# Performance work log

Hardware: AMD Instinct MI355X
Metric: run time of the kernel (lower is better)

Reference implementation:

```python
import jax, jax.numpy as jnp
import numpy as np

# Graph layout: B equal-sized graphs, contiguous node ids.
B, NG, EG = 64, 2000, 64000          # graphs, nodes/graph, edges/graph
K = 1600                              # ceil(0.8 * NG) — TopKPooling ratio=0.8
N, E = B * NG, B * EG
FEAT_DIM, EMB, G1, G2, DENSE, NCLS = 10000, 64, 32, 32, 64, 10


def setup_inputs() -> dict:
    key = jax.random.key(0)
    ks = jax.random.split(key, 12)
    x = jax.random.randint(ks[0], (N, 1), 0, FEAT_DIM)
    # random edges within each graph, then offset by graph base node id
    e = jax.random.randint(ks[1], (2, B, EG), 0, NG) + (jnp.arange(B) * NG)[None, :, None]
    edge_index = e.reshape(2, E)
    batch = jnp.repeat(jnp.arange(B), NG)
    sc = 0.05
    return {
        "x": x, "edge_index": edge_index, "batch": batch,
        "emb": jax.random.normal(ks[2], (FEAT_DIM, EMB), jnp.float32) * sc,
        "W1": jax.random.normal(ks[3], (EMB, G1), jnp.float32) * sc,
        "b1": jnp.zeros((G1,), jnp.float32),
        "W2": jax.random.normal(ks[4], (G1, G2), jnp.float32) * sc,
        "b2": jnp.zeros((G2,), jnp.float32),
        "pool_w": jax.random.normal(ks[5], (G2,), jnp.float32) * sc,
        "dense_W": jax.random.normal(ks[6], (G2, DENSE), jnp.float32) * sc,
        "dense_b": jnp.zeros((DENSE,), jnp.float32),
        "out_W": jax.random.normal(ks[7], (DENSE, NCLS), jnp.float32) * sc,
        "out_b": jnp.zeros((NCLS,), jnp.float32),
    }


def gcn_layer(h, src, dst, W, b):
    """PyG GCNConv: add self-loops, symmetric D^-1/2 A D^-1/2 aggregation."""
    n = h.shape[0]
    loop = jnp.arange(n)
    s = jnp.concatenate([src, loop])
    d = jnp.concatenate([dst, loop])
    h = h @ W                                                   # [N, out]
    deg = jax.ops.segment_sum(jnp.ones_like(d, dtype=h.dtype), d, num_segments=n)
    dinv = jnp.where(deg > 0, deg ** -0.5, 0.0)
    norm = dinv[s] * dinv[d]                                    # [E+N]
    out = jax.ops.segment_sum(h[s] * norm[:, None], d, num_segments=n)
    return out + b


def reference(x, edge_index, batch, emb, W1, b1, W2, b2, pool_w,
              dense_W, dense_b, out_W, out_b):
    h = emb[x[:, 0]]                                            # [N, EMB]
    src, dst = edge_index[0], edge_index[1]
    h = jax.nn.relu(gcn_layer(h, src, dst, W1, b1))
    h = jax.nn.relu(gcn_layer(h, src, dst, W2, b2))
    # TopKPooling: score = tanh(x.w / ||w||); keep top ceil(0.8*NG) per graph,
    # scale kept features by their scores. Equal graph sizes -> static shapes.
    score = jnp.tanh(h @ pool_w / jnp.linalg.norm(pool_w))      # [N]
    sb = score.reshape(B, NG)
    hb = h.reshape(B, NG, G2)
    vals, idx = jax.lax.top_k(sb, K)                            # [B, K]
    hp = jnp.take_along_axis(hb, idx[:, :, None], axis=1) * vals[:, :, None]
    g = hp.max(axis=1)                                          # global max pool [B, G2]
    d = jax.nn.relu(g @ dense_W + dense_b)
    return d @ out_W + out_b                                    # [B, NCLS]
```

## Files before the change

### kernel.cpp

```cpp
#include <hip/hip_runtime.h>
#include <hip/hip_fp16.h>
#include <math.h>

#define NB 64
#define NGRAPH 2000
#define EGRAPH 64000
#define NN (NB*NGRAPH)
#define NE (NB*EGRAPH)
#define KSEL 1600
#define FEAT 10000
#define EMBD 64
#define G1D 32
#define G2D 32
#define DENSED 64
#define NCLSD 10
#define NCHUNK 8
#define CHUNK_E (EGRAPH/NCHUNK)
#define NQD 8
#define QNODES (NGRAPH/NQD)
#define LOUT_CAP 10000
#define AGG_PARTS 4
#define NPP (NGRAPH/AGG_PARTS)


__device__ __forceinline__ float4 ld_row8h(const char* base, unsigned byteoff)
{
    uint2 u = *(const uint2*)(base + byteoff);
    __half2 p0 = *(__half2*)&u.x;
    __half2 p1 = *(__half2*)&u.y;
    float2 f0 = __half22float2(p0);
    float2 f1 = __half22float2(p1);
    return make_float4(f0.x, f0.y, f1.x, f1.y);
}

__device__ __forceinline__ void st_row8h(__half* dst, float4 v)
{
    __half2 p0 = __floats2half2_rn(v.x, v.y);
    __half2 p1 = __floats2half2_rn(v.z, v.w);
    uint2 u;
    u.x = *(unsigned*)&p0;
    u.y = *(unsigned*)&p1;
    *(uint2*)dst = u;
}

__global__ __launch_bounds__(256) void prep_kernel(const int* __restrict__ ei,
                                                   int* __restrict__ chist,
                                                   const float* __restrict__ emb,
                                                   const float* __restrict__ W1,
                                                   float* __restrict__ embW)
{
    __shared__ float shmem[2048];
    const int tid = threadIdx.x;
    if (blockIdx.x < 512) {
        int* hist = (int*)shmem;
        const int lb = blockIdx.x;
        const int xcd = lb & 7, t = lb >> 3;
        const int g = xcd * 8 + (t >> 3);
        const int q = t & 7;
        const int base_e = g * EGRAPH + q * CHUNK_E;
        const int base_n = g * NGRAPH;
        for (int v = tid; v < NGRAPH; v += 256) hist[v] = 0;
        __syncthreads();
        for (int k = tid; k < CHUNK_E; k += 256) {
            int d = ei[NE + base_e + k];
            atomicAdd(&hist[d - base_n], 1);
        }
        __syncthreads();
        int* out = chist + (size_t)(g * NCHUNK + q) * NGRAPH;
        for (int v = tid; v < NGRAPH; v += 256) out[v] = hist[v];
    } else {
        float* W1s = shmem;
        for (int i = tid; i < EMBD * G1D; i += 256) W1s[i] = W1[i];
        __syncthreads();
        int id = (blockIdx.x - 512) * 256 + tid;
        int r = id >> 5, c = id & 31;
        if (r >= FEAT) return;
        const float* er = emb + r * EMBD;
        float acc = 0.f;
        #pragma unroll 8
        for (int k = 0; k < EMBD; ++k) acc += er[k] * W1s[k * G1D + c];
        embW[r * G1D + c] = acc;
    }
}

__global__ __launch_bounds__(256) void scan_graph(const int* __restrict__ chist,
                                                  float* __restrict__ dinv,
                                                  int* __restrict__ row_start)
{
    __shared__ int hist[NGRAPH];
    __shared__ int csA[256];
    __shared__ int csB[256];
    const int b = (blockIdx.x & 7) * 8 + (blockIdx.x >> 3);
    const int tid = threadIdx.x;
    const int base_n = b * NGRAPH, base_e = b * EGRAPH;
    const int* ch = chist + (size_t)b * NCHUNK * NGRAPH;

    for (int v = tid; v < NGRAPH; v += 256) {
        int tot = 0;
        #pragma unroll
        for (int q = 0; q < NCHUNK; ++q) tot += ch[q * NGRAPH + v];
        hist[v] = tot;
        dinv[base_n + v] = rsqrtf((float)(tot + 1));
    }
    __syncthreads();
    if (tid < 250) {
        int s = 0;
        #pragma unroll
        for (int i = 0; i < 8; ++i) s += hist[tid * 8 + i];
        csA[tid] = s;
    }
    __syncthreads();
    int* sb = csA; int* db = csB;
    for (int off = 1; off < 256; off <<= 1) {
        int v = 0;
        if (tid < 250) { v = sb[tid]; if (tid >= off) v += sb[tid - off]; }
        if (tid < 250) db[tid] = v;
        __syncthreads();
        int* t = sb; sb = db; db = t;
    }
    if (tid < 250) {
        int run = (tid == 0) ? 0 : sb[tid - 1];
        #pragma unroll
        for (int i = 0; i < 8; ++i) {
            int idx = tid * 8 + i;
            int c = hist[idx];
            row_start[base_n + idx] = base_e + run;
            run += c;
        }
    }
}

__global__ __launch_bounds__(1024) void mid_kernel(const int* __restrict__ ei,
                                                   const int* __restrict__ row_start,
                                                   int* __restrict__ csr,
                                                   const int* __restrict__ x,
                                                   const float* __restrict__ embW,
                                                   const float* __restrict__ dinv,
                                                   __half* __restrict__ A)
{
    __shared__ int cur[QNODES];
    __shared__ int lout[LOUT_CAP];
    const int tid = threadIdx.x;
    if (blockIdx.x < 512) {
        const int lb = blockIdx.x;
        const int xcd = lb & 7, t = lb >> 3;
        const int g = xcd * 8 + (t >> 3);
        const int qd = t & 7;
        const int base_n = g * NGRAPH;
        const int lo = qd * QNODES;
        const int base = row_start[base_n + lo];
        const int qend = (g == NB - 1 && qd == NQD - 1) ? NE
                         : row_start[base_n + lo + QNODES];
        for (int v = tid; v < QNODES; v += 1024)
            cur[v] = row_start[base_n + lo + v] - base;
        __syncthreads();
        const int4* srcp = (const int4*)(ei + g * EGRAPH);
        const int4* dstp = (const int4*)(ei + NE + g * EGRAPH);
        const int sub = base_n + lo;
        for (int k = tid; k < EGRAPH / 4; k += 1024) {
            int4 d4 = dstp[k];
            int4 s4 = srcp[k];
            int d, pos;
            d = d4.x - sub;
            if ((unsigned)d < (unsigned)QNODES) {
                pos = atomicAdd(&cur[d], 1);
                if (pos < LOUT_CAP) lout[pos] = s4.x << 6;
            }
            d = d4.y - sub;
            if ((unsigned)d < (unsigned)QNODES) {
                pos = atomicAdd(&cur[d], 1);
                if (pos < LOUT_CAP) lout[pos] = s4.y << 6;
            }
            d = d4.z - sub;
            if ((unsigned)d < (unsigned)QNODES) {
                pos = atomicAdd(&cur[d], 1);
                if (pos < LOUT_CAP) lout[pos] = s4.z << 6;
            }
            d = d4.w - sub;
            if ((unsigned)d < (unsigned)QNODES) {
                pos = atomicAdd(&cur[d], 1);
                if (pos < LOUT_CAP) lout[pos] = s4.w << 6;
            }
        }
        __syncthreads();
        int size = qend - base;
        if (size > LOUT_CAP) size = LOUT_CAP;
        for (int i = tid; i < size; i += 1024)
            csr[base + i] = lout[i];
    } else {
        int id = (blockIdx.x - 512) * 1024 + tid;
        int v = id >> 3, r = id & 7;
        int xv = x[v];
        float dv = dinv[v];
        float4 e = ((const float4*)(embW + (size_t)xv * G1D))[r];
        e.x *= dv; e.y *= dv; e.z *= dv; e.w *= dv;
        st_row8h(A + (size_t)v * G1D + r * 4, e);
    }
}


__global__ __launch_bounds__(1024) void agg1_kernel(const __half* __restrict__ Ain,
                                                    const float* __restrict__ dinv,
                                                    const int* __restrict__ row_start,
                                                    const int* __restrict__ csr,
                                                    const float* __restrict__ b1,
                                                    const float* __restrict__ W2,
                                                    __half* __restrict__ Bout)
{
    __shared__ uint4 table4[NGRAPH * 4];
    __shared__ float hsh[32][G2D];
    const int lb = blockIdx.x;
    const int xcd = lb & 7, t = lb >> 3;
    const int b = xcd * 8 + (t >> 2);
    const int part = t & 3;
    const int tid = threadIdx.x;
    const int base_n = b * NGRAPH;
    const int boff = base_n << 6;

    {
        const uint4* src = (const uint4*)(Ain + (size_t)base_n * G1D);
        for (int i = tid; i < NGRAPH * 4; i += 1024) table4[i] = src[i];
    }
    __syncthreads();

    const char* Lbase = (const char*)table4;
    const int hw = tid >> 5;
    const int hl = tid & 31;
    const int slot = hl >> 3;
    const int r = hl & 7;
    const int roff = r << 3;
    const float4 bias4 = ((const float4*)b1)[r];

    float w2c[G1D];
    #pragma unroll
    for (int k = 0; k < G1D; ++k) w2c[k] = W2[k * G2D + hl];

    const int vloc0 = part * NPP + hw * 16;
    const int vend = part * NPP + NPP;
    int v = base_n + vloc0;
    int rs = row_start[v];
    int re = (v == NN - 1) ? NE : row_start[v + 1];
    int s0 = csr[rs + slot] - boff;
    int s1 = csr[rs + slot + 4] - boff;
    int s2 = csr[rs + slot + 8] - boff;
    int s3 = csr[rs + slot + 12] - boff;

    for (int i = 0; i < 16; ++i) {
        int vloc = vloc0 + i;
        if (vloc >= vend) break;
        int re_next = (v + 1 >= NN - 1) ? NE : row_start[v + 2];
        int n0 = csr[re + slot] - boff;
        int n1 = csr[re + slot + 4] - boff;
        int n2 = csr[re + slot + 8] - boff;
        int n3 = csr[re + slot + 12] - boff;

        int me = rs + ((re - rs) & ~15);
        float4 acc0 = make_float4(0.f, 0.f, 0.f, 0.f);
        float4 acc1 = make_float4(0.f, 0.f, 0.f, 0.f);
        float4 acc2 = make_float4(0.f, 0.f, 0.f, 0.f);
        float4 acc3 = make_float4(0.f, 0.f, 0.f, 0.f);
        if (slot == 0)
            acc0 = ld_row8h(Lbase, (unsigned)((vloc << 6) + roff));
        int j = rs + slot;
        while (j < me) {
            int jn = j + 16;
            int t0 = csr[jn] - boff;
            int t1 = csr[jn + 4] - boff;
            int t2 = csr[jn + 8] - boff;
            int t3 = csr[jn + 12] - boff;
            float4 a0 = ld_row8h(Lbase, (unsigned)(s0 + roff));
            float4 a1 = ld_row8h(Lbase, (unsigned)(s1 + roff));
            float4 a2 = ld_row8h(Lbase, (unsigned)(s2 + roff));
            float4 a3 = ld_row8h(Lbase, (unsigned)(s3 + roff));
            acc0.x += a0.x; acc0.y += a0.y; acc0.z += a0.z; acc0.w += a0.w;
            acc1.x += a1.x; acc1.y += a1.y; acc1.z += a1.z; acc1.w += a1.w;
            acc2.x += a2.x; acc2.y += a2.y; acc2.z += a2.z; acc2.w += a2.w;
            acc3.x += a3.x; acc3.y += a3.y; acc3.z += a3.z; acc3.w += a3.w;
            j = jn; s0 = t0; s1 = t1; s2 = t2; s3 = t3;
        }
        {
            int jt = me + slot;
            if (jt < re) {
                float4 a = ld_row8h(Lbase, (unsigned)(s0 + roff));
                acc0.x += a.x; acc0.y += a.y; acc0.z += a.z; acc0.w += a.w;
            }
            if (jt + 4 < re) {
                float4 a = ld_row8h(Lbase, (unsigned)(s1 + roff));
                acc1.x += a.x; acc1.y += a.y; acc1.z += a.z; acc1.w += a.w;
            }
            if (jt + 8 < re) {
                float4 a = ld_row8h(Lbase, (unsigned)(s2 + roff));
                acc2.x += a.x; acc2.y += a.y; acc2.z += a.z; acc2.w += a.w;
            }
            if (jt + 12 < re) {
                float4 a = ld_row8h(Lbase, (unsigned)(s3 + roff));
                acc3.x += a.x; acc3.y += a.y; acc3.z += a.z; acc3.w += a.w;
            }
        }
        float4 acc;
        acc.x = (acc0.x + acc1.x) + (acc2.x + acc3.x);
        acc.y = (acc0.y + acc1.y) + (acc2.y + acc3.y);
        acc.z = (acc0.z + acc1.z) + (acc2.z + acc3.z);
        acc.w = (acc0.w + acc1.w) + (acc2.w + acc3.w);
        #pragma unroll
        for (int off = 8; off <= 16; off <<= 1) {
            acc.x += __shfl_xor(acc.x, off, 32);
            acc.y += __shfl_xor(acc.y, off, 32);
            acc.z += __shfl_xor(acc.z, off, 32);
            acc.w += __shfl_xor(acc.w, off, 32);
        }
        float dv = dinv[v];
        if (slot == 0) {
            float4 h4;
            h4.x = fmaxf(dv * acc.x + bias4.x, 0.f);
            h4.y = fmaxf(dv * acc.y + bias4.y, 0.f);
            h4.z = fmaxf(dv * acc.z + bias4.z, 0.f);
            h4.w = fmaxf(dv * acc.w + bias4.w, 0.f);
            ((float4*)&hsh[hw][0])[r] = h4;
        }
        float o0 = 0.f, o1 = 0.f, o2 = 0.f, o3 = 0.f;
        const float4* hrow = (const float4*)&hsh[hw][0];
        #pragma unroll
        for (int q = 0; q < 8; ++q) {
            float4 hh = hrow[q];
            o0 += hh.x * w2c[4 * q + 0];
            o1 += hh.y * w2c[4 * q + 1];
            o2 += hh.z * w2c[4 * q + 2];
            o3 += hh.w * w2c[4 * q + 3];
        }
        Bout[(size_t)v * G2D + hl] = __float2half(dv * ((o0 + o1) + (o2 + o3)));
        v = v + 1;
        rs = re; re = re_next; s0 = n0; s1 = n1; s2 = n2; s3 = n3;
    }
}

__global__ __launch_bounds__(1024) void agg2_kernel(const __half* __restrict__ Bin,
                                                    const float* __restrict__ dinv,
                                                    const int* __restrict__ row_start,
                                                    const int* __restrict__ csr,
                                                    const float* __restrict__ b2,
                                                    const float* __restrict__ pool_w,
                                                    __half* __restrict__ h2out,
                                                    float* __restrict__ scores)
{
    __shared__ uint4 table4[NGRAPH * 4];
    const int lb = blockIdx.x;
    const int xcd = lb & 7, t = lb >> 3;
    const int b = xcd * 8 + (t >> 2);
    const int part = t & 3;
    const int tid = threadIdx.x;
    const int base_n = b * NGRAPH;
    const int boff = base_n << 6;

    {
        const uint4* src = (const uint4*)(Bin + (size_t)base_n * G1D);
        for (int i = tid; i < NGRAPH * 4; i += 1024) table4[i] = src[i];
    }
    __syncthreads();

    const char* Lbase = (const char*)table4;
    const int hw = tid >> 5;
    const int hl = tid & 31;
    const int slot = hl >> 3;
    const int r = hl & 7;
    const int roff = r << 3;
    const float4 bias4 = ((const float4*)b2)[r];
    const float4 pw4 = ((const float4*)pool_w)[r];

    float pw = pool_w[hl];
    float nsq = pw * pw;
    #pragma unroll
    for (int off = 16; off; off >>= 1) nsq += __shfl_xor(nsq, off, 32);
    const float inv_norm = rsqrtf(nsq);

    const int vloc0 = part * NPP + hw * 16;
    const int vend = part * NPP + NPP;
    int v = base_n + vloc0;
    int rs = row_start[v];
    int re = (v == NN - 1) ? NE : row_start[v + 1];
    int s0 = csr[rs + slot] - boff;
    int s1 = csr[rs + slot + 4] - boff;
    int s2 = csr[rs + slot + 8] - boff;
    int s3 = csr[rs + slot + 12] - boff;

    for (int i = 0; i < 16; ++i) {
        int vloc = vloc0 + i;
        if (vloc >= vend) break;
        int re_next = (v + 1 >= NN - 1) ? NE : row_start[v + 2];
        int n0 = csr[re + slot] - boff;
        int n1 = csr[re + slot + 4] - boff;
        int n2 = csr[re + slot + 8] - boff;
        int n3 = csr[re + slot + 12] - boff;

        int me = rs + ((re - rs) & ~15);
        float4 acc0 = make_float4(0.f, 0.f, 0.f, 0.f);
        float4 acc1 = make_float4(0.f, 0.f, 0.f, 0.f);
        float4 acc2 = make_float4(0.f, 0.f, 0.f, 0.f);
        float4 acc3 = make_float4(0.f, 0.f, 0.f, 0.f);
        if (slot == 0)
            acc0 = ld_row8h(Lbase, (unsigned)((vloc << 6) + roff));
        int j = rs + slot;
        while (j < me) {
            int jn = j + 16;
            int t0 = csr[jn] - boff;
            int t1 = csr[jn + 4] - boff;
            int t2 = csr[jn + 8] - boff;
            int t3 = csr[jn + 12] - boff;
            float4 a0 = ld_row8h(Lbase, (unsigned)(s0 + roff));
            float4 a1 = ld_row8h(Lbase, (unsigned)(s1 + roff));
            float4 a2 = ld_row8h(Lbase, (unsigned)(s2 + roff));
            float4 a3 = ld_row8h(Lbase, (unsigned)(s3 + roff));
            acc0.x += a0.x; acc0.y += a0.y; acc0.z += a0.z; acc0.w += a0.w;
            acc1.x += a1.x; acc1.y += a1.y; acc1.z += a1.z; acc1.w += a1.w;
            acc2.x += a2.x; acc2.y += a2.y; acc2.z += a2.z; acc2.w += a2.w;
            acc3.x += a3.x; acc3.y += a3.y; acc3.z += a3.z; acc3.w += a3.w;
            j = jn; s0 = t0; s1 = t1; s2 = t2; s3 = t3;
        }
        {
            int jt = me + slot;
            if (jt < re) {
                float4 a = ld_row8h(Lbase, (unsigned)(s0 + roff));
                acc0.x += a.x; acc0.y += a.y; acc0.z += a.z; acc0.w += a.w;
            }
            if (jt + 4 < re) {
                float4 a = ld_row8h(Lbase, (unsigned)(s1 + roff));
                acc1.x += a.x; acc1.y += a.y; acc1.z += a.z; acc1.w += a.w;
            }
            if (jt + 8 < re) {
                float4 a = ld_row8h(Lbase, (unsigned)(s2 + roff));
                acc2.x += a.x; acc2.y += a.y; acc2.z += a.z; acc2.w += a.w;
            }
            if (jt + 12 < re) {
                float4 a = ld_row8h(Lbase, (unsigned)(s3 + roff));
                acc3.x += a.x; acc3.y += a.y; acc3.z += a.z; acc3.w += a.w;
            }
        }
        float4 acc;
        acc.x = (acc0.x + acc1.x) + (acc2.x + acc3.x);
        acc.y = (acc0.y + acc1.y) + (acc2.y + acc3.y);
        acc.z = (acc0.z + acc1.z) + (acc2.z + acc3.z);
        acc.w = (acc0.w + acc1.w) + (acc2.w + acc3.w);
        #pragma unroll
        for (int off = 8; off <= 16; off <<= 1) {
            acc.x += __shfl_xor(acc.x, off, 32);
            acc.y += __shfl_xor(acc.y, off, 32);
            acc.z += __shfl_xor(acc.z, off, 32);
            acc.w += __shfl_xor(acc.w, off, 32);
        }
        float dv = dinv[v];
        float4 h4;
        h4.x = fmaxf(dv * acc.x + bias4.x, 0.f);
        h4.y = fmaxf(dv * acc.y + bias4.y, 0.f);
        h4.z = fmaxf(dv * acc.z + bias4.z, 0.f);
        h4.w = fmaxf(dv * acc.w + bias4.w, 0.f);
        if (slot == 0)
            st_row8h(h2out + (size_t)v * G2D + r * 4, h4);
        float tt = h4.x * pw4.x + h4.y * pw4.y + h4.z * pw4.z + h4.w * pw4.w;
        tt += __shfl_xor(tt, 1, 32);
        tt += __shfl_xor(tt, 2, 32);
        tt += __shfl_xor(tt, 4, 32);
        if (hl == 0) scores[v] = tanhf(tt * inv_norm);
        v = v + 1;
        rs = re; re = re_next; s0 = n0; s1 = n1; s2 = n2; s3 = n3;
    }
}

__global__ __launch_bounds__(256) void topk_pool_mlp(const __half* __restrict__ h2,
                                                     const float* __restrict__ scores,
                                                     const float* __restrict__ dense_W,
                                                     const float* __restrict__ dense_b,
                                                     const float* __restrict__ out_W,
                                                     const float* __restrict__ out_b,
                                                     float* __restrict__ out)
{
    __shared__ unsigned keys[NGRAPH];
    __shared__ float    sval[NGRAPH];
    __shared__ unsigned char inc[NGRAPH];
    __shared__ int  hist[256];
    __shared__ int  csA[256];
    __shared__ int  csB[256];
    __shared__ int  sel[2];
    __shared__ int  redc[4];
    __shared__ float redf[32][32];
    __shared__ float gvec[32];
    __shared__ float dvec[DENSED];
    const int b = (blockIdx.x & 7) * 8 + (blockIdx.x >> 3);
    const int tid = threadIdx.x;
    const int base_n = b * NGRAPH;

    for (int v = tid; v < NGRAPH; v += 256) {
        float f = scores[base_n + v];
        sval[v] = f;
        unsigned u = __float_as_uint(f);
        keys[v] = (u & 0x80000000u) ? ~u : (u | 0x80000000u);
    }
    __syncthreads();

    unsigned T = 0;
    int need = KSEL;
    #pragma unroll
    for (int pass = 0; pass < 4; ++pass) {
        const int s = 24 - pass * 8;
        const unsigned hi_mask = (pass == 0) ? 0u : (0xFFFFFFFFu << (s + 8));
        hist[tid] = 0;
        __syncthreads();
        for (int v = tid; v < NGRAPH; v += 256) {
            unsigned k = keys[v];
            if ((k & hi_mask) == (T & hi_mask))
                atomicAdd(&hist[(k >> s) & 255], 1);
        }
        __syncthreads();
        csA[tid] = hist[255 - tid];
        __syncthreads();
        int* sb = csA; int* db = csB;
        for (int off = 1; off < 256; off <<= 1) {
            int val = sb[tid];
            if (tid >= off) val += sb[tid - off];
            db[tid] = val;
            __syncthreads();
            int* t = sb; sb = db; db = t;
        }
        {
            const int d = tid;
            int suf_d = sb[255 - d];
            int suf_d1 = (d == 255) ? 0 : sb[254 - d];
            if (suf_d >= need && suf_d1 < need) {
                sel[0] = d;
                sel[1] = suf_d1;
            }
        }
        __syncthreads();
        T |= ((unsigned)sel[0]) << s;
        need -= sel[1];
        __syncthreads();
    }

    const int wid = tid >> 6, ln = tid & 63;
    int cg = 0, ce = 0;
    for (int v = tid; v < NGRAPH; v += 256) {
        cg += (keys[v] > T) ? 1 : 0;
        ce += (keys[v] == T) ? 1 : 0;
    }
    int packed = (cg << 16) | ce;
    #pragma unroll
    for (int off = 32; off; off >>= 1) packed += __shfl_down(packed, off, 64);
    if (ln == 0) redc[wid] = packed;
    __syncthreads();
    int tot = redc[0] + redc[1] + redc[2] + redc[3];
    int m_gt = tot >> 16, m_eq = tot & 0xffff;
    int needed = KSEL - m_gt;
    float fT = (T & 0x80000000u) ? __uint_as_float(T & 0x7fffffffu)
                                 : __uint_as_float(~T);
    if (m_eq == needed || fT == 0.0f) {
        for (int v = tid; v < NGRAPH; v += 256) inc[v] = (keys[v] >= T) ? 1 : 0;
    } else {
        if (tid == 0) {
            int take = 0;
            for (int v = 0; v < NGRAPH; ++v) {
                unsigned k = keys[v];
                if (k > T) inc[v] = 1;
                else if (k == T && take < needed) { inc[v] = 1; ++take; }
                else inc[v] = 0;
            }
        }
    }
    __syncthreads();

    {
        const int rowslot = tid >> 3;
        const int c4 = tid & 7;
        float4 m4 = make_float4(-INFINITY, -INFINITY, -INFINITY, -INFINITY);
        const char* h2base = (const char*)h2;
        for (int v = rowslot; v < NGRAPH; v += 32) {
            float4 hrow = ld_row8h(h2base,
                                   (unsigned)((base_n + v) * (G2D * 2) + c4 * 8));
            float sv = inc[v] ? sval[v] : 0.f;
            float big = inc[v] ? 0.f : -INFINITY;
            m4.x = fmaxf(m4.x, sv * hrow.x + big);
            m4.y = fmaxf(m4.y, sv * hrow.y + big);
            m4.z = fmaxf(m4.z, sv * hrow.z + big);
            m4.w = fmaxf(m4.w, sv * hrow.w + big);
        }
        redf[rowslot][c4 * 4 + 0] = m4.x;
        redf[rowslot][c4 * 4 + 1] = m4.y;
        redf[rowslot][c4 * 4 + 2] = m4.z;
        redf[rowslot][c4 * 4 + 3] = m4.w;
    }
    __syncthreads();
    if (tid < 32) {
        float g = redf[0][tid];
        #pragma unroll
        for (int rr = 1; rr < 32; ++rr) g = fmaxf(g, redf[rr][tid]);
        gvec[tid] = g;
    }
    __syncthreads();
    if (tid < DENSED) {
        float t = dense_b[tid];
        #pragma unroll
        for (int k = 0; k < G2D; ++k) t += gvec[k] * dense_W[k * DENSED + tid];
        dvec[tid] = fmaxf(t, 0.f);
    }
    __syncthreads();
    if (tid < NCLSD) {
        float o = out_b[tid];
        #pragma unroll
        for (int j = 0; j < DENSED; ++j) o += dvec[j] * out_W[j * NCLSD + tid];
        out[b * NCLSD + tid] = o;
    }
}

extern "C" void kernel_launch(void* const* d_in, const int* in_sizes, int n_in,
                              void* d_out, int out_size, void* d_ws, size_t ws_size,
                              hipStream_t stream)
{
    (void)in_sizes; (void)n_in; (void)out_size; (void)ws_size;
    const int*   x       = (const int*)  d_in[0];
    const int*   edge    = (const int*)  d_in[1];
    const float* emb     = (const float*)d_in[3];
    const float* W1      = (const float*)d_in[4];
    const float* b1      = (const float*)d_in[5];
    const float* W2      = (const float*)d_in[6];
    const float* b2      = (const float*)d_in[7];
    const float* pool_w  = (const float*)d_in[8];
    const float* dense_W = (const float*)d_in[9];
    const float* dense_b = (const float*)d_in[10];
    const float* out_W   = (const float*)d_in[11];
    const float* out_b   = (const float*)d_in[12];
    float* outp = (float*)d_out;

    char* ws = (char*)d_ws;
    float*  embW      = (float*)ws;
    __half* Ah        = (__half*)(ws + 1280000);
    __half* Bh        = (__half*)(ws + 1280000 + 8192000);
    float*  dinv      = (float*)(ws + 1280000 + 2*8192000);
    int*    row_start = (int*)((char*)dinv + (size_t)NN*4);
    int*    csr       = (int*)((char*)row_start + (size_t)NN*4);
    float*  scores    = (float*)((char*)csr + (size_t)(NE+16)*4);

    int* chist = (int*)Bh;

    prep_kernel<<<512 + (FEAT * G1D) / 256, 256, 0, stream>>>(edge, chist, emb, W1, embW);
    scan_graph<<<NB, 256, 0, stream>>>(chist, dinv, row_start);
    mid_kernel<<<512 + (NN * 8) / 1024, 1024, 0, stream>>>(edge, row_start, csr,
                                                           x, embW, dinv, Ah);
    agg1_kernel<<<NB * AGG_PARTS, 1024, 0, stream>>>(Ah, dinv, row_start, csr, b1, W2, Bh);
    agg2_kernel<<<NB * AGG_PARTS, 1024, 0, stream>>>(Bh, dinv, row_start, csr, b2, pool_w, Ah, scores);
    topk_pool_mlp<<<NB, 256, 0, stream>>>(Ah, scores, dense_W, dense_b, out_W, out_b, outp);
}
```

Measured before the change: 226.0 us.

## Pad shared node table rows, store graph-local offsets, accumulate in half2

```diff
diff --git a/kernel.cpp b/kernel.cpp
--- a/kernel.cpp
+++ b/kernel.cpp
@@ -21,6 +21,7 @@
 #define LOUT_CAP 10000
 #define AGG_PARTS 4
 #define NPP (NGRAPH/AGG_PARTS)
+#define RSTRIDE 72
 
 
 __device__ __forceinline__ float4 ld_row8h(const char* base, unsigned byteoff)
@@ -41,6 +42,21 @@
     u.x = *(unsigned*)&p0;
     u.y = *(unsigned*)&p1;
     *(uint2*)dst = u;
+}
+
+__device__ __forceinline__ void acc8h(const char* base, unsigned off,
+                                      __half2& lo, __half2& hi)
+{
+    uint2 u = *(const uint2*)(base + off);
+    lo = __hadd2(lo, *(__half2*)&u.x);
+    hi = __hadd2(hi, *(__half2*)&u.y);
+}
+
+__device__ __forceinline__ float4 h2tof4(__half2 lo, __half2 hi)
+{
+    float2 a = __half22float2(lo);
+    float2 b = __half22float2(hi);
+    return make_float4(a.x, a.y, b.x, b.y);
 }
 
 __global__ __launch_bounds__(256) void prep_kernel(const int* __restrict__ ei,
@@ -160,26 +176,30 @@
         for (int k = tid; k < EGRAPH / 4; k += 1024) {
             int4 d4 = dstp[k];
             int4 s4 = srcp[k];
-            int d, pos;
+            int d, pos, sl;
             d = d4.x - sub;
             if ((unsigned)d < (unsigned)QNODES) {
                 pos = atomicAdd(&cur[d], 1);
-                if (pos < LOUT_CAP) lout[pos] = s4.x << 6;
+                sl = s4.x - base_n;
+                if (pos < LOUT_CAP) lout[pos] = (sl << 6) + (sl << 3);
             }
             d = d4.y - sub;
             if ((unsigned)d < (unsigned)QNODES) {
                 pos = atomicAdd(&cur[d], 1);
-                if (pos < LOUT_CAP) lout[pos] = s4.y << 6;
+                sl = s4.y - base_n;
+                if (pos < LOUT_CAP) lout[pos] = (sl << 6) + (sl << 3);
             }
             d = d4.z - sub;
             if ((unsigned)d < (unsigned)QNODES) {
                 pos = atomicAdd(&cur[d], 1);
-                if (pos < LOUT_CAP) lout[pos] = s4.z << 6;
+                sl = s4.z - base_n;
+                if (pos < LOUT_CAP) lout[pos] = (sl << 6) + (sl << 3);
             }
             d = d4.w - sub;
             if ((unsigned)d < (unsigned)QNODES) {
                 pos = atomicAdd(&cur[d], 1);
-                if (pos < LOUT_CAP) lout[pos] = s4.w << 6;
+                sl = s4.w - base_n;
+                if (pos < LOUT_CAP) lout[pos] = (sl << 6) + (sl << 3);
             }
         }
         __syncthreads();
@@ -207,7 +227,7 @@
                                                     const float* __restrict__ W2,
                                                     __half* __restrict__ Bout)
 {
-    __shared__ uint4 table4[NGRAPH * 4];
+    __shared__ uint2 table2[NGRAPH * 9];
     __shared__ float hsh[32][G2D];
     const int lb = blockIdx.x;
     const int xcd = lb & 7, t = lb >> 3;
@@ -215,15 +235,15 @@
     const int part = t & 3;
     const int tid = threadIdx.x;
     const int base_n = b * NGRAPH;
-    const int boff = base_n << 6;
 
     {
-        const uint4* src = (const uint4*)(Ain + (size_t)base_n * G1D);
-        for (int i = tid; i < NGRAPH * 4; i += 1024) table4[i] = src[i];
-    }
-    __syncthreads();
-
-    const char* Lbase = (const char*)table4;
+        const uint2* src = (const uint2*)(Ain + (size_t)base_n * G1D);
+        for (int i = tid; i < NGRAPH * 8; i += 1024)
+            table2[(i >> 3) * 9 + (i & 7)] = src[i];
+    }
+    __syncthreads();
+
+    const char* Lbase = (const char*)table2;
     const int hw = tid >> 5;
     const int hl = tid & 31;
     const int slot = hl >> 3;
@@ -235,73 +255,61 @@
     #pragma unroll
     for (int k = 0; k < G1D; ++k) w2c[k] = W2[k * G2D + hl];
 
+    const __half2 z2 = __float2half2_rn(0.f);
+
     const int vloc0 = part * NPP + hw * 16;
     const int vend = part * NPP + NPP;
     int v = base_n + vloc0;
     int rs = row_start[v];
     int re = (v == NN - 1) ? NE : row_start[v + 1];
-    int s0 = csr[rs + slot] - boff;
-    int s1 = csr[rs + slot + 4] - boff;
-    int s2 = csr[rs + slot + 8] - boff;
-    int s3 = csr[rs + slot + 12] - boff;
+    int s0 = csr[rs + slot];
+    int s1 = csr[rs + slot + 4];
+    int s2 = csr[rs + slot + 8];
+    int s3 = csr[rs + slot + 12];
 
     for (int i = 0; i < 16; ++i) {
         int vloc = vloc0 + i;
         if (vloc >= vend) break;
         int re_next = (v + 1 >= NN - 1) ? NE : row_start[v + 2];
-        int n0 = csr[re + slot] - boff;
-        int n1 = csr[re + slot + 4] - boff;
-        int n2 = csr[re + slot + 8] - boff;
-        int n3 = csr[re + slot + 12] - boff;
+        int n0 = csr[re + slot];
+        int n1 = csr[re + slot + 4];
+        int n2 = csr[re + slot + 8];
+        int n3 = csr[re + slot + 12];
 
         int me = rs + ((re - rs) & ~15);
-        float4 acc0 = make_float4(0.f, 0.f, 0.f, 0.f);
-        float4 acc1 = make_float4(0.f, 0.f, 0.f, 0.f);
-        float4 acc2 = make_float4(0.f, 0.f, 0.f, 0.f);
-        float4 acc3 = make_float4(0.f, 0.f, 0.f, 0.f);
+        __half2 l0 = z2, h0 = z2, l1 = z2, h1 = z2;
+        __half2 l2 = z2, h2 = z2, l3 = z2, h3 = z2;
         if (slot == 0)
-            acc0 = ld_row8h(Lbase, (unsigned)((vloc << 6) + roff));
+            acc8h(Lbase, (unsigned)((vloc << 6) + (vloc << 3) + roff), l0, h0);
         int j = rs + slot;
         while (j < me) {
             int jn = j + 16;
-            int t0 = csr[jn] - boff;
-            int t1 = csr[jn + 4] - boff;
-            int t2 = csr[jn + 8] - boff;
-            int t3 = csr[jn + 12] - boff;
-            float4 a0 = ld_row8h(Lbase, (unsigned)(s0 + roff));
-            float4 a1 = ld_row8h(Lbase, (unsigned)(s1 + roff));
-            float4 a2 = ld_row8h(Lbase, (unsigned)(s2 + roff));
-            float4 a3 = ld_row8h(Lbase, (unsigned)(s3 + roff));
-            acc0.x += a0.x; acc0.y += a0.y; acc0.z += a0.z; acc0.w += a0.w;
-            acc1.x += a1.x; acc1.y += a1.y; acc1.z += a1.z; acc1.w += a1.w;
-            acc2.x += a2.x; acc2.y += a2.y; acc2.z += a2.z; acc2.w += a2.w;
-            acc3.x += a3.x; acc3.y += a3.y; acc3.z += a3.z; acc3.w += a3.w;
+            int t0 = csr[jn];
+            int t1 = csr[jn + 4];
+            int t2 = csr[jn + 8];
+            int t3 = csr[jn + 12];
+            acc8h(Lbase, (unsigned)(s0 + roff), l0, h0);
+            acc8h(Lbase, (unsigned)(s1 + roff), l1, h1);
+            acc8h(Lbase, (unsigned)(s2 + roff), l2, h2);
+            acc8h(Lbase, (unsigned)(s3 + roff), l3, h3);
             j = jn; s0 = t0; s1 = t1; s2 = t2; s3 = t3;
         }
         {
             int jt = me + slot;
-            if (jt < re) {
-                float4 a = ld_row8h(Lbase, (unsigned)(s0 + roff));
-                acc0.x += a.x; acc0.y += a.y; acc0.z += a.z; acc0.w += a.w;
-            }
-            if (jt + 4 < re) {
-                float4 a = ld_row8h(Lbase, (unsigned)(s1 + roff));
-                acc1.x += a.x; acc1.y += a.y; acc1.z += a.z; acc1.w += a.w;
-            }
-            if (jt + 8 < re) {
-                float4 a = ld_row8h(Lbase, (unsigned)(s2 + roff));
-                acc2.x += a.x; acc2.y += a.y; acc2.z += a.z; acc2.w += a.w;
-            }
-            if (jt + 12 < re) {
-                float4 a = ld_row8h(Lbase, (unsigned)(s3 + roff));
-                acc3.x += a.x; acc3.y += a.y; acc3.z += a.z; acc3.w += a.w;
-            }
-        }
+            if (jt < re)      acc8h(Lbase, (unsigned)(s0 + roff), l0, h0);
+            if (jt + 4 < re)  acc8h(Lbase, (unsigned)(s1 + roff), l1, h1);
+            if (jt + 8 < re)  acc8h(Lbase, (unsigned)(s2 + roff), l2, h2);
+            if (jt + 12 < re) acc8h(Lbase, (unsigned)(s3 + roff), l3, h3);
+        }
+        float4 f0 = h2tof4(l0, h0);
+        float4 f1 = h2tof4(l1, h1);
+        float4 f2 = h2tof4(l2, h2);
+        float4 f3 = h2tof4(l3, h3);
         float4 acc;
-        acc.x = (acc0.x + acc1.x) + (acc2.x + acc3.x);
-        acc.y = (acc0.y + acc1.y) + (acc2.y + acc3.y);
-        acc.z = (acc0.z + acc1.z) + (acc2.z + acc3.z);
-        acc.w = (acc0.w + acc1.w) + (acc2.w + acc3.w);
+        acc.x = (f0.x + f1.x) + (f2.x + f3.x);
+        acc.y = (f0.y + f1.y) + (f2.y + f3.y);
+        acc.z = (f0.z + f1.z) + (f2.z + f3.z);
+        acc.w = (f0.w + f1.w) + (f2.w + f3.w);
         #pragma unroll
         for (int off = 8; off <= 16; off <<= 1) {
             acc.x += __shfl_xor(acc.x, off, 32);
@@ -343,22 +351,22 @@
                                                     __half* __restrict__ h2out,
                                                     float* __restrict__ scores)
 {
-    __shared__ uint4 table4[NGRAPH * 4];
+    __shared__ uint2 table2[NGRAPH * 9];
     const int lb = blockIdx.x;
     const int xcd = lb & 7, t = lb >> 3;
     const int b = xcd * 8 + (t >> 2);
     const int part = t & 3;
     const int tid = threadIdx.x;
     const int base_n = b * NGRAPH;
-    const int boff = base_n << 6;
 
     {
-        const uint4* src = (const uint4*)(Bin + (size_t)base_n * G1D);
-        for (int i = tid; i < NGRAPH * 4; i += 1024) table4[i] = src[i];
-    }
-    __syncthreads();
-
-    const char* Lbase = (const char*)table4;
+        const uint2* src = (const uint2*)(Bin + (size_t)base_n * G1D);
+        for (int i = tid; i < NGRAPH * 8; i += 1024)
+            table2[(i >> 3) * 9 + (i & 7)] = src[i];
+    }
+    __syncthreads();
+
+    const char* Lbase = (const char*)table2;
     const int hw = tid >> 5;
     const int hl = tid & 31;
     const int slot = hl >> 3;
@@ -373,73 +381,61 @@
     for (int off = 16; off; off >>= 1) nsq += __shfl_xor(nsq, off, 32);
     const float inv_norm = rsqrtf(nsq);
 
+    const __half2 z2 = __float2half2_rn(0.f);
+
     const int vloc0 = part * NPP + hw * 16;
     const int vend = part * NPP + NPP;
     int v = base_n + vloc0;
     int rs = row_start[v];
     int re = (v == NN - 1) ? NE : row_start[v + 1];
-    int s0 = csr[rs + slot] - boff;
-    int s1 = csr[rs + slot + 4] - boff;
-    int s2 = csr[rs + slot + 8] - boff;
-    int s3 = csr[rs + slot + 12] - boff;
+    int s0 = csr[rs + slot];
+    int s1 = csr[rs + slot + 4];
+    int s2 = csr[rs + slot + 8];
+    int s3 = csr[rs + slot + 12];
 
     for (int i = 0; i < 16; ++i) {
         int vloc = vloc0 + i;
         if (vloc >= vend) break;
         int re_next = (v + 1 >= NN - 1) ? NE : row_start[v + 2];
-        int n0 = csr[re + slot] - boff;
-        int n1 = csr[re + slot + 4] - boff;
-        int n2 = csr[re + slot + 8] - boff;
-        int n3 = csr[re + slot + 12] - boff;
+        int n0 = csr[re + slot];
+        int n1 = csr[re + slot + 4];
+        int n2 = csr[re + slot + 8];
+        int n3 = csr[re + slot + 12];
 
         int me = rs + ((re - rs) & ~15);
-        float4 acc0 = make_float4(0.f, 0.f, 0.f, 0.f);
-        float4 acc1 = make_float4(0.f, 0.f, 0.f, 0.f);
-        float4 acc2 = make_float4(0.f, 0.f, 0.f, 0.f);
-        float4 acc3 = make_float4(0.f, 0.f, 0.f, 0.f);
+        __half2 l0 = z2, h0 = z2, l1 = z2, h1 = z2;
+        __half2 l2 = z2, h2 = z2, l3 = z2, h3 = z2;
         if (slot == 0)
-            acc0 = ld_row8h(Lbase, (unsigned)((vloc << 6) + roff));
+            acc8h(Lbase, (unsigned)((vloc << 6) + (vloc << 3) + roff), l0, h0);
         int j = rs + slot;
         while (j < me) {
             int jn = j + 16;
-            int t0 = csr[jn] - boff;
-            int t1 = csr[jn + 4] - boff;
-            int t2 = csr[jn + 8] - boff;
-            int t3 = csr[jn + 12] - boff;
-            float4 a0 = ld_row8h(Lbase, (unsigned)(s0 + roff));
-            float4 a1 = ld_row8h(Lbase, (unsigned)(s1 + roff));
-            float4 a2 = ld_row8h(Lbase, (unsigned)(s2 + roff));
-            float4 a3 = ld_row8h(Lbase, (unsigned)(s3 + roff));
-            acc0.x += a0.x; acc0.y += a0.y; acc0.z += a0.z; acc0.w += a0.w;
-            acc1.x += a1.x; acc1.y += a1.y; acc1.z += a1.z; acc1.w += a1.w;
-            acc2.x += a2.x; acc2.y += a2.y; acc2.z += a2.z; acc2.w += a2.w;
-            acc3.x += a3.x; acc3.y += a3.y; acc3.z += a3.z; acc3.w += a3.w;
+            int t0 = csr[jn];
+            int t1 = csr[jn + 4];
+            int t2 = csr[jn + 8];
+            int t3 = csr[jn + 12];
+            acc8h(Lbase, (unsigned)(s0 + roff), l0, h0);
+            acc8h(Lbase, (unsigned)(s1 + roff), l1, h1);
+            acc8h(Lbase, (unsigned)(s2 + roff), l2, h2);
+            acc8h(Lbase, (unsigned)(s3 + roff), l3, h3);
             j = jn; s0 = t0; s1 = t1; s2 = t2; s3 = t3;
         }
         {
             int jt = me + slot;
-            if (jt < re) {
-                float4 a = ld_row8h(Lbase, (unsigned)(s0 + roff));
-                acc0.x += a.x; acc0.y += a.y; acc0.z += a.z; acc0.w += a.w;
-            }
-            if (jt + 4 < re) {
-                float4 a = ld_row8h(Lbase, (unsigned)(s1 + roff));
-                acc1.x += a.x; acc1.y += a.y; acc1.z += a.z; acc1.w += a.w;
-            }
-            if (jt + 8 < re) {
-                float4 a = ld_row8h(Lbase, (unsigned)(s2 + roff));
-                acc2.x += a.x; acc2.y += a.y; acc2.z += a.z; acc2.w += a.w;
-            }
-            if (jt + 12 < re) {
-                float4 a = ld_row8h(Lbase, (unsigned)(s3 + roff));
-                acc3.x += a.x; acc3.y += a.y; acc3.z += a.z; acc3.w += a.w;
-            }
-        }
+            if (jt < re)      acc8h(Lbase, (unsigned)(s0 + roff), l0, h0);
+            if (jt + 4 < re)  acc8h(Lbase, (unsigned)(s1 + roff), l1, h1);
+            if (jt + 8 < re)  acc8h(Lbase, (unsigned)(s2 + roff), l2, h2);
+            if (jt + 12 < re) acc8h(Lbase, (unsigned)(s3 + roff), l3, h3);
+        }
+        float4 f0 = h2tof4(l0, h0);
+        float4 f1 = h2tof4(l1, h1);
+        float4 f2 = h2tof4(l2, h2);
+        float4 f3 = h2tof4(l3, h3);
         float4 acc;
-        acc.x = (acc0.x + acc1.x) + (acc2.x + acc3.x);
-        acc.y = (acc0.y + acc1.y) + (acc2.y + acc3.y);
-        acc.z = (acc0.z + acc1.z) + (acc2.z + acc3.z);
-        acc.w = (acc0.w + acc1.w) + (acc2.w + acc3.w);
+        acc.x = (f0.x + f1.x) + (f2.x + f3.x);
+        acc.y = (f0.y + f1.y) + (f2.y + f3.y);
+        acc.z = (f0.z + f1.z) + (f2.z + f3.z);
+        acc.w = (f0.w + f1.w) + (f2.w + f3.w);
         #pragma unroll
         for (int off = 8; off <= 16; off <<= 1) {
             acc.x += __shfl_xor(acc.x, off, 32);
```

After: 224.7 us. No clear change (-0.6%).
